# Optimization experiments

Hardware: AMD Instinct MI355X
Metric: run time of the kernel (lower is better)

## Reference

```python
import jax, jax.numpy as jnp
import numpy as np

N, E, D = 50000, 800000, 256

def setup_inputs() -> dict:
    key = jax.random.key(0)
    ks = jax.random.split(key, 12)
    s = 1.0 / np.sqrt(D)
    return {
        "x": jax.random.normal(ks[0], (N, D), dtype=jnp.float32),
        "src": jax.random.randint(ks[1], (E,), 0, N, dtype=jnp.int64),
        "dst": jax.random.randint(ks[2], (E,), 0, N, dtype=jnp.int64),
        "W_w": jax.random.normal(ks[3], (D, D), dtype=jnp.float32) * s,
        "W_b": jnp.zeros((D,), dtype=jnp.float32),
        "U_w": jax.random.normal(ks[4], (D, D), dtype=jnp.float32) * s,
        "U_b": jnp.zeros((D,), dtype=jnp.float32),
        "V_w": jax.random.normal(ks[5], (D, D), dtype=jnp.float32) * s,
        "V_b": jnp.zeros((D,), dtype=jnp.float32),
        "attn_l": jax.random.normal(ks[6], (D,), dtype=jnp.float32) * s,
        "attn_r": jax.random.normal(ks[7], (D,), dtype=jnp.float32) * s,
        "gamma": jnp.ones((D,), dtype=jnp.float32),
        "beta": jnp.zeros((D,), dtype=jnp.float32),
    }

def reference(x, src, dst, W_w, W_b, U_w, U_b, V_w, V_b, attn_l, attn_r, gamma, beta):
    # node transforms (dropout p=0 -> identity)
    Wh = x @ W_w + W_b            # [N, D]
    Uh = x @ U_w + U_b            # [N, D]
    Vh = x @ V_w + V_b            # [N, D]
    out_src = Wh * attn_l         # [N, D]
    out_dst = Wh * attn_r         # [N, D]
    # per-edge gate: sigma = sigmoid(out_src[u] + out_dst[v])  [E, D]
    sigma = jax.nn.sigmoid(out_src[src] + out_dst[dst])
    # aggregate to destination nodes
    sum_sigma_h = jax.ops.segment_sum(Vh[src] * sigma, dst, num_segments=N)
    sum_sigma = jax.ops.segment_sum(sigma, dst, num_segments=N)
    h = Uh + sum_sigma_h / (sum_sigma + 1e-6)
    # layer norm (eps=1e-6, affine)
    mu = jnp.mean(h, axis=-1, keepdims=True)
    var = jnp.mean((h - mu) ** 2, axis=-1, keepdims=True)
    h = (h - mu) / jnp.sqrt(var + 1e-6) * gamma + beta
    h = jax.nn.relu(h)
    return x + h  # residual
```

## Files before the change

### kernel.cpp

```cpp
#include <hip/hip_runtime.h>
#include <hip/hip_bf16.h>

#define NN 50000
#define NE 800000
#define NB 196

typedef __attribute__((ext_vector_type(8))) short short8;
typedef __attribute__((ext_vector_type(4))) float floatx4;
typedef unsigned short u16;
typedef unsigned int u32;

__device__ __forceinline__ u16 f2bf(float f) {
    u32 u = __float_as_uint(f);
    u += 0x7FFFu + ((u >> 16) & 1u);
    return (u16)(u >> 16);
}
__device__ __forceinline__ float bf_lo(u32 u) { return __uint_as_float(u << 16); }
__device__ __forceinline__ float bf_hi(u32 u) { return __uint_as_float(u & 0xFFFF0000u); }
__device__ __forceinline__ u32 pack_bf(float lo, float hi) {
    return (u32)f2bf(lo) | ((u32)f2bf(hi) << 16);
}
__device__ __forceinline__ void gl_lds16(const void* g, void* l) {
    __builtin_amdgcn_global_load_lds((const __attribute__((address_space(1))) void*)g,
                                     (__attribute__((address_space(3))) void*)l, 16, 0, 0);
}

__global__ __launch_bounds__(256) void tw_kernel(const float* __restrict__ W, const float* __restrict__ U,
                                                 const float* __restrict__ V, u16* __restrict__ wT) {
    __shared__ float s[32][33];
    int g = blockIdx.z;
    const float* M = (g == 0) ? W : ((g == 1) ? U : V);
    int r0 = blockIdx.x * 32, c0 = blockIdx.y * 32;
    int tx = threadIdx.x & 31, ty = threadIdx.x >> 5;
#pragma unroll
    for (int k = 0; k < 4; ++k)
        s[ty + k * 8][tx] = M[(size_t)(r0 + ty + k * 8) * 256 + c0 + tx];
    __syncthreads();
#pragma unroll
    for (int k = 0; k < 4; ++k)
        wT[(size_t)(g * 256 + c0 + ty + k * 8) * 256 + r0 + tx] = f2bf(s[tx][ty + k * 8]);
}

__global__ void hist_kernel(const int* __restrict__ dst, int* __restrict__ deg) {
    int e = blockIdx.x * 256 + threadIdx.x;
    if (e < NE) atomicAdd(&deg[dst[e]], 1);
}

__global__ __launch_bounds__(256) void scanA_kernel(const int* __restrict__ deg, int* __restrict__ bsum) {
    int t = threadIdx.x;
    int i = blockIdx.x * 256 + t;
    int v = (i < NN) ? deg[i] : 0;
#pragma unroll
    for (int m = 32; m; m >>= 1) v += __shfl_xor(v, m, 64);
    __shared__ int ws[4];
    if ((t & 63) == 0) ws[t >> 6] = v;
    __syncthreads();
    if (t == 0) bsum[blockIdx.x] = ws[0] + ws[1] + ws[2] + ws[3];
}

__global__ __launch_bounds__(256) void scanB_kernel(const int* __restrict__ bsum, int* __restrict__ bpre,
                                                    int* __restrict__ rows_end) {
    int t = threadIdx.x, lane = t & 63, wv = t >> 6;
    int v = (t < NB) ? bsum[t] : 0;
    int inc = v;
#pragma unroll
    for (int off = 1; off < 64; off <<= 1) {
        int u = __shfl_up(inc, off, 64);
        if (lane >= off) inc += u;
    }
    __shared__ int wsum[4];
    if (lane == 63) wsum[wv] = inc;
    __syncthreads();
    int woff = 0;
    for (int k = 0; k < wv; ++k) woff += wsum[k];
    if (t < NB) bpre[t] = woff + inc - v;
    if (t == 255) rows_end[0] = woff + inc;
}

__global__ __launch_bounds__(256) void scanC_kernel(const int* __restrict__ deg, const int* __restrict__ bpre,
                                                    int* __restrict__ rows, int* __restrict__ cursor) {
    int t = threadIdx.x, lane = t & 63, wv = t >> 6;
    int i = blockIdx.x * 256 + t;
    int v = (i < NN) ? deg[i] : 0;
    int inc = v;
#pragma unroll
    for (int off = 1; off < 64; off <<= 1) {
        int u = __shfl_up(inc, off, 64);
        if (lane >= off) inc += u;
    }
    __shared__ int wsum[4];
    if (lane == 63) wsum[wv] = inc;
    __syncthreads();
    int woff = bpre[blockIdx.x];
    for (int k = 0; k < wv; ++k) woff += wsum[k];
    int excl = woff + inc - v;
    if (i < NN) { rows[i] = excl; cursor[i] = excl; }
}

__global__ void scatter_kernel(const int* __restrict__ src, const int* __restrict__ dst,
                               int* __restrict__ cursor, int* __restrict__ esrc) {
    int e = blockIdx.x * 256 + threadIdx.x;
    if (e < NE) {
        int d = dst[e];
        int pos = atomicAdd(&cursor[d], 1);
        esrc[pos] = src[e];
    }
}

__global__ __launch_bounds__(256) void gemm_kernel(
    const float* __restrict__ x, const u16* __restrict__ wT,
    const float* __restrict__ Wb, const float* __restrict__ Ub, const float* __restrict__ Vb,
    u16* __restrict__ WVh, float* __restrict__ Uh) {
    __shared__ __align__(16) u16 As[128 * 64];
    __shared__ __align__(16) u16 Bs[128 * 64];

    int rb = blockIdx.x * 128;
    int cbg = blockIdx.y * 128;
    int t = threadIdx.x, lane = t & 63, w = t >> 6;
    int wm = w >> 1, wn = w & 1;

    floatx4 acc[4][4] = {};

    int b_subrow = lane >> 3;
    int b_q = lane & 7;
    int a_row = t >> 1;
    int a_half = t & 1;

    for (int kt = 0; kt < 4; ++kt) {
        int k0 = kt * 64;
#pragma unroll
        for (int ii = 0; ii < 4; ++ii) {
            int rowbase = (w * 4 + ii) * 8;
            int row = rowbase + b_subrow;
            int qa = b_q ^ (row & 7);
            gl_lds16(wT + (size_t)(cbg + row) * 256 + k0 + qa * 8, Bs + rowbase * 64);
        }
        int grow = rb + a_row;
        uint4 pk[4] = {};
        if (grow < NN) {
            const float* px = x + (size_t)grow * 256 + k0 + a_half * 32;
#pragma unroll
            for (int c = 0; c < 4; ++c) {
                floatx4 f0 = *(const floatx4*)(px + c * 8);
                floatx4 f1 = *(const floatx4*)(px + c * 8 + 4);
                pk[c].x = pack_bf(f0[0], f0[1]);
                pk[c].y = pack_bf(f0[2], f0[3]);
                pk[c].z = pack_bf(f1[0], f1[1]);
                pk[c].w = pack_bf(f1[2], f1[3]);
            }
        }
#pragma unroll
        for (int c = 0; c < 4; ++c) {
            int q = a_half * 4 + c;
            *(uint4*)(As + a_row * 64 + ((q ^ (a_row & 7)) * 8)) = pk[c];
        }
        __syncthreads();

#pragma unroll
        for (int s = 0; s < 2; ++s) {
            short8 a[4], b[4];
#pragma unroll
            for (int i = 0; i < 4; ++i) {
                int ar = wm * 64 + i * 16 + (lane & 15);
                int q = s * 4 + (lane >> 4);
                a[i] = *(const short8*)(As + ar * 64 + ((q ^ (ar & 7)) * 8));
                int br = wn * 64 + i * 16 + (lane & 15);
                b[i] = *(const short8*)(Bs + br * 64 + ((q ^ (br & 7)) * 8));
            }
#pragma unroll
            for (int i = 0; i < 4; ++i)
#pragma unroll
                for (int j = 0; j < 4; ++j)
                    acc[i][j] = __builtin_amdgcn_mfma_f32_16x16x32_bf16(a[i], b[j], acc[i][j], 0, 0, 0);
        }
        __syncthreads();
    }

    int g = cbg >> 8;
    int cloc = cbg & 255;
    const float* bias = (g == 0) ? Wb : ((g == 1) ? Ub : Vb);
#pragma unroll
    for (int i = 0; i < 4; ++i)
#pragma unroll
        for (int j = 0; j < 4; ++j) {
            int col = cloc + wn * 64 + j * 16 + (lane & 15);
            float bv = bias[col];
#pragma unroll
            for (int r = 0; r < 4; ++r) {
                int row = rb + wm * 64 + i * 16 + (lane >> 4) * 4 + r;
                if (row < NN) {
                    float val = acc[i][j][r] + bv;
                    if (g == 0)      WVh[(size_t)row * 512 + col] = f2bf(val);
                    else if (g == 1) Uh[(size_t)row * 256 + col] = val;
                    else             WVh[(size_t)row * 512 + 256 + col] = f2bf(val);
                }
            }
        }
}

__global__ __launch_bounds__(256) void node_kernel(
    const u16* __restrict__ WVh, const float* __restrict__ x,
    const int* __restrict__ rows, const int* __restrict__ esrc,
    const float* __restrict__ attn_l, const float* __restrict__ attn_r,
    const float* __restrict__ gamma, const float* __restrict__ beta,
    float* inout) {
    int wv = threadIdx.x >> 6, lane = threadIdx.x & 63;
    int v = blockIdx.x * 4 + wv;
    if (v >= NN) return;
    int c0 = lane * 4;

    floatx4 al = *(const floatx4*)(attn_l + c0);
    floatx4 ar = *(const floatx4*)(attn_r + c0);

    uint2 wvv = *(const uint2*)(WVh + (size_t)v * 512 + c0);
    float td[4] = { bf_lo(wvv.x) * ar[0], bf_hi(wvv.x) * ar[1],
                    bf_lo(wvv.y) * ar[2], bf_hi(wvv.y) * ar[3] };

    float acc_h[4] = {0.f, 0.f, 0.f, 0.f};
    float acc_s[4] = {0.f, 0.f, 0.f, 0.f};

    int e0 = rows[v], e1 = rows[v + 1];
    for (int e = e0; e < e1; ++e) {
        int u = esrc[e];
        const u16* base = WVh + (size_t)u * 512 + c0;
        uint2 wu = *(const uint2*)(base);
        uint2 vu = *(const uint2*)(base + 256);
        float wf[4] = { bf_lo(wu.x), bf_hi(wu.x), bf_lo(wu.y), bf_hi(wu.y) };
        float vf[4] = { bf_lo(vu.x), bf_hi(vu.x), bf_lo(vu.y), bf_hi(vu.y) };
#pragma unroll
        for (int j = 0; j < 4; ++j) {
            float tt = fmaf(wf[j], al[j], td[j]);
            float s = __builtin_amdgcn_rcpf(1.0f + __expf(-tt));
            acc_s[j] += s;
            acc_h[j] = fmaf(s, vf[j], acc_h[j]);
        }
    }

    floatx4 uh = *(const floatx4*)(inout + (size_t)v * 256 + c0);
    float h[4];
#pragma unroll
    for (int j = 0; j < 4; ++j)
        h[j] = uh[j] + acc_h[j] * __builtin_amdgcn_rcpf(acc_s[j] + 1e-6f);

    float s01 = h[0] + h[1] + h[2] + h[3];
#pragma unroll
    for (int m = 32; m; m >>= 1) s01 += __shfl_xor(s01, m, 64);
    float mu = s01 * (1.0f / 256.0f);
    float d[4] = { h[0] - mu, h[1] - mu, h[2] - mu, h[3] - mu };
    float sq = d[0] * d[0] + d[1] * d[1] + d[2] * d[2] + d[3] * d[3];
#pragma unroll
    for (int m = 32; m; m >>= 1) sq += __shfl_xor(sq, m, 64);
    float inv = rsqrtf(sq * (1.0f / 256.0f) + 1e-6f);

    floatx4 gm = *(const floatx4*)(gamma + c0);
    floatx4 bt = *(const floatx4*)(beta + c0);
    floatx4 xr = *(const floatx4*)(x + (size_t)v * 256 + c0);
    floatx4 res;
#pragma unroll
    for (int j = 0; j < 4; ++j) {
        float y = d[j] * inv * gm[j] + bt[j];
        y = fmaxf(y, 0.0f);
        res[j] = xr[j] + y;
    }
    *(floatx4*)(inout + (size_t)v * 256 + c0) = res;
}

extern "C" void kernel_launch(void* const* d_in, const int* in_sizes, int n_in,
                              void* d_out, int out_size, void* d_ws, size_t ws_size,
                              hipStream_t stream) {
    const float* x       = (const float*)d_in[0];
    const int*   src     = (const int*)d_in[1];
    const int*   dst     = (const int*)d_in[2];
    const float* W_w     = (const float*)d_in[3];
    const float* W_b     = (const float*)d_in[4];
    const float* U_w     = (const float*)d_in[5];
    const float* U_b     = (const float*)d_in[6];
    const float* V_w     = (const float*)d_in[7];
    const float* V_b     = (const float*)d_in[8];
    const float* attn_l  = (const float*)d_in[9];
    const float* attn_r  = (const float*)d_in[10];
    const float* gamma   = (const float*)d_in[11];
    const float* beta    = (const float*)d_in[12];

    char* ws = (char*)d_ws;
    size_t off = 0;
    auto alloc = [&](size_t bytes) -> char* {
        char* p = ws + off;
        off += (bytes + 255) & ~(size_t)255;
        return p;
    };
    u16* WVh     = (u16*)alloc((size_t)NN * 512 * 2);
    u16* wT      = (u16*)alloc((size_t)768 * 256 * 2);
    int* deg     = (int*)alloc((size_t)NN * 4);
    int* rows    = (int*)alloc((size_t)(NN + 1) * 4);
    int* cursor  = (int*)alloc((size_t)NN * 4);
    int* esrc    = (int*)alloc((size_t)NE * 4);
    int* bsum    = (int*)alloc((size_t)NB * 4);
    int* bpre    = (int*)alloc((size_t)NB * 4);

    float* Uh_f32 = (float*)d_out;

    hipMemsetAsync(deg, 0, (size_t)NN * 4, stream);

    tw_kernel<<<dim3(8, 8, 3), 256, 0, stream>>>(W_w, U_w, V_w, wT);
    hist_kernel<<<(NE + 255) / 256, 256, 0, stream>>>(dst, deg);
    scanA_kernel<<<NB, 256, 0, stream>>>(deg, bsum);
    scanB_kernel<<<1, 256, 0, stream>>>(bsum, bpre, rows + NN);
    scanC_kernel<<<NB, 256, 0, stream>>>(deg, bpre, rows, cursor);
    scatter_kernel<<<(NE + 255) / 256, 256, 0, stream>>>(src, dst, cursor, esrc);

    dim3 gg((NN + 127) / 128, 6);
    gemm_kernel<<<gg, 256, 0, stream>>>(x, wT, W_b, U_b, V_b, WVh, Uh_f32);

    node_kernel<<<(NN + 3) / 4, 256, 0, stream>>>(
        WVh, x, rows, esrc, attn_l, attn_r, gamma, beta, (float*)d_out);
}
```

Before: 339.3 us.

## Pre-convert x to bf16 for direct LDS loads and unroll edge gather

Adds a kernel that converts x to bf16 in a padded workspace buffer. The GEMM can then load A tiles straight into LDS with global_load_lds, the same way it loads the weights, instead of loading fp32 through registers and converting. It keeps the old fp32 GEMM as a fallback when the workspace is too small. Separately, the node kernel's edge loop is unrolled by four so several gathers are in flight at once, and the sigmoid argument is negated ahead of the loop. The cost is an extra pass over x plus a launch, and rows past NN in the padded buffer are read without being initialised.

```diff
diff --git a/kernel.cpp b/kernel.cpp
--- a/kernel.cpp
+++ b/kernel.cpp
@@ -4,6 +4,7 @@
 #define NN 50000
 #define NE 800000
 #define NB 196
+#define NROWPAD 50048
 
 typedef __attribute__((ext_vector_type(8))) short short8;
 typedef __attribute__((ext_vector_type(4))) float floatx4;
@@ -23,6 +24,18 @@
 __device__ __forceinline__ void gl_lds16(const void* g, void* l) {
     __builtin_amdgcn_global_load_lds((const __attribute__((address_space(1))) void*)g,
                                      (__attribute__((address_space(3))) void*)l, 16, 0, 0);
+}
+
+__global__ __launch_bounds__(256) void xcvt_kernel(const float* __restrict__ x, u16* __restrict__ xbf) {
+    size_t i = (size_t)(blockIdx.x * 256 + threadIdx.x) * 8;
+    floatx4 f0 = *(const floatx4*)(x + i);
+    floatx4 f1 = *(const floatx4*)(x + i + 4);
+    uint4 pk;
+    pk.x = pack_bf(f0[0], f0[1]);
+    pk.y = pack_bf(f0[2], f0[3]);
+    pk.z = pack_bf(f1[0], f1[1]);
+    pk.w = pack_bf(f1[2], f1[3]);
+    *(uint4*)(xbf + i) = pk;
 }
 
 __global__ __launch_bounds__(256) void tw_kernel(const float* __restrict__ W, const float* __restrict__ U,
@@ -107,7 +120,78 @@
     }
 }
 
-__global__ __launch_bounds__(256) void gemm_kernel(
+__global__ __launch_bounds__(256) void gemm_bf_kernel(
+    const u16* __restrict__ xbf, const u16* __restrict__ wT,
+    const float* __restrict__ Wb, const float* __restrict__ Ub, const float* __restrict__ Vb,
+    u16* __restrict__ WVh, float* __restrict__ Uh) {
+    __shared__ __align__(16) u16 As[128 * 64];
+    __shared__ __align__(16) u16 Bs[128 * 64];
+
+    int rb = blockIdx.x * 128;
+    int cbg = blockIdx.y * 128;
+    int t = threadIdx.x, lane = t & 63, w = t >> 6;
+    int wm = w >> 1, wn = w & 1;
+
+    floatx4 acc[4][4] = {};
+
+    int subrow = lane >> 3;
+    int qv = lane & 7;
+
+    for (int kt = 0; kt < 4; ++kt) {
+        int k0 = kt * 64;
+#pragma unroll
+        for (int ii = 0; ii < 4; ++ii) {
+            int rowbase = (w * 4 + ii) * 8;
+            int row = rowbase + subrow;
+            int qa = qv ^ (row & 7);
+            gl_lds16(wT + (size_t)(cbg + row) * 256 + k0 + qa * 8, Bs + rowbase * 64);
+            gl_lds16(xbf + (size_t)(rb + row) * 256 + k0 + qa * 8, As + rowbase * 64);
+        }
+        __syncthreads();
+
+#pragma unroll
+        for (int s = 0; s < 2; ++s) {
+            short8 a[4], b[4];
+#pragma unroll
+            for (int i = 0; i < 4; ++i) {
+                int ar = wm * 64 + i * 16 + (lane & 15);
+                int q = s * 4 + (lane >> 4);
+                a[i] = *(const short8*)(As + ar * 64 + ((q ^ (ar & 7)) * 8));
+                int br = wn * 64 + i * 16 + (lane & 15);
+                b[i] = *(const short8*)(Bs + br * 64 + ((q ^ (br & 7)) * 8));
+            }
+#pragma unroll
+            for (int i = 0; i < 4; ++i)
+#pragma unroll
+                for (int j = 0; j < 4; ++j)
+                    acc[i][j] = __builtin_amdgcn_mfma_f32_16x16x32_bf16(a[i], b[j], acc[i][j], 0, 0, 0);
+        }
+        __syncthreads();
+    }
+
+    int g = cbg >> 8;
+    int cloc = cbg & 255;
+    const float* bias = (g == 0) ? Wb : ((g == 1) ? Ub : Vb);
+#pragma unroll
+    for (int i = 0; i < 4; ++i)
+#pragma unroll
+        for (int j = 0; j < 4; ++j) {
+            int col = cloc + wn * 64 + j * 16 + (lane & 15);
+            float bv = bias[col];
+#pragma unroll
+            for (int r = 0; r < 4; ++r) {
+                int row = rb + wm * 64 + i * 16 + (lane >> 4) * 4 + r;
+                if (row < NN) {
+                    float val = acc[i][j][r] + bv;
+                    if (g == 0)      WVh[(size_t)row * 512 + col] = f2bf(val);
+                    else if (g == 1) Uh[(size_t)row * 256 + col] = val;
+                    else             WVh[(size_t)row * 512 + 256 + col] = f2bf(val);
+                }
+            }
+        }
+}
+
+__global__ __launch_bounds__(256) void gemm_f32_kernel(
     const float* __restrict__ x, const u16* __restrict__ wT,
     const float* __restrict__ Wb, const float* __restrict__ Ub, const float* __restrict__ Vb,
     u16* __restrict__ WVh, float* __restrict__ Uh) {
@@ -120,7 +204,6 @@
     int wm = w >> 1, wn = w & 1;
 
     floatx4 acc[4][4] = {};
-
     int b_subrow = lane >> 3;
     int b_q = lane & 7;
     int a_row = t >> 1;
@@ -209,31 +292,46 @@
     if (v >= NN) return;
     int c0 = lane * 4;
 
-    floatx4 al = *(const floatx4*)(attn_l + c0);
-    floatx4 ar = *(const floatx4*)(attn_r + c0);
-
+    floatx4 alv = *(const floatx4*)(attn_l + c0);
+    floatx4 arv = *(const floatx4*)(attn_r + c0);
     uint2 wvv = *(const uint2*)(WVh + (size_t)v * 512 + c0);
-    float td[4] = { bf_lo(wvv.x) * ar[0], bf_hi(wvv.x) * ar[1],
-                    bf_lo(wvv.y) * ar[2], bf_hi(wvv.y) * ar[3] };
+    float al2[4] = { -alv[0], -alv[1], -alv[2], -alv[3] };
+    float td2[4] = { -bf_lo(wvv.x) * arv[0], -bf_hi(wvv.x) * arv[1],
+                     -bf_lo(wvv.y) * arv[2], -bf_hi(wvv.y) * arv[3] };
 
     float acc_h[4] = {0.f, 0.f, 0.f, 0.f};
     float acc_s[4] = {0.f, 0.f, 0.f, 0.f};
 
-    int e0 = rows[v], e1 = rows[v + 1];
-    for (int e = e0; e < e1; ++e) {
-        int u = esrc[e];
-        const u16* base = WVh + (size_t)u * 512 + c0;
-        uint2 wu = *(const uint2*)(base);
-        uint2 vu = *(const uint2*)(base + 256);
+    auto edge = [&](uint2 wu, uint2 vu) {
         float wf[4] = { bf_lo(wu.x), bf_hi(wu.x), bf_lo(wu.y), bf_hi(wu.y) };
         float vf[4] = { bf_lo(vu.x), bf_hi(vu.x), bf_lo(vu.y), bf_hi(vu.y) };
 #pragma unroll
         for (int j = 0; j < 4; ++j) {
-            float tt = fmaf(wf[j], al[j], td[j]);
-            float s = __builtin_amdgcn_rcpf(1.0f + __expf(-tt));
+            float m = fmaf(wf[j], al2[j], td2[j]);
+            float s = __builtin_amdgcn_rcpf(1.0f + __expf(m));
             acc_s[j] += s;
             acc_h[j] = fmaf(s, vf[j], acc_h[j]);
         }
+    };
+
+    int e = rows[v], e1 = rows[v + 1];
+    for (; e + 4 <= e1; e += 4) {
+        int ua = esrc[e], ub = esrc[e + 1], uc = esrc[e + 2], ud = esrc[e + 3];
+        const u16* pa = WVh + (size_t)ua * 512 + c0;
+        const u16* pb = WVh + (size_t)ub * 512 + c0;
+        const u16* pc = WVh + (size_t)uc * 512 + c0;
+        const u16* pd = WVh + (size_t)ud * 512 + c0;
+        uint2 wa = *(const uint2*)pa, va = *(const uint2*)(pa + 256);
+        uint2 wb = *(const uint2*)pb, vb = *(const uint2*)(pb + 256);
+        uint2 wc = *(const uint2*)pc, vc = *(const uint2*)(pc + 256);
+        uint2 wd = *(const uint2*)pd, vd = *(const uint2*)(pd + 256);
+        edge(wa, va); edge(wb, vb); edge(wc, vc); edge(wd, vd);
+    }
+    for (; e < e1; ++e) {
+        int u = esrc[e];
+        const u16* p = WVh + (size_t)u * 512 + c0;
+        uint2 wu = *(const uint2*)p, vu = *(const uint2*)(p + 256);
+        edge(wu, vu);
     }
 
     floatx4 uh = *(const floatx4*)(inout + (size_t)v * 256 + c0);
@@ -297,6 +395,8 @@
     int* esrc    = (int*)alloc((size_t)NE * 4);
     int* bsum    = (int*)alloc((size_t)NB * 4);
     int* bpre    = (int*)alloc((size_t)NB * 4);
+    u16* xbf     = (u16*)alloc((size_t)NROWPAD * 256 * 2);
+    bool use_bf  = (ws_size >= off);
 
     float* Uh_f32 = (float*)d_out;
 
@@ -310,7 +410,12 @@
     scatter_kernel<<<(NE + 255) / 256, 256, 0, stream>>>(src, dst, cursor, esrc);
 
     dim3 gg((NN + 127) / 128, 6);
-    gemm_kernel<<<gg, 256, 0, stream>>>(x, wT, W_b, U_b, V_b, WVh, Uh_f32);
+    if (use_bf) {
+        xcvt_kernel<<<(NN * 256 / 8 + 255) / 256, 256, 0, stream>>>(x, xbf);
+        gemm_bf_kernel<<<gg, 256, 0, stream>>>(xbf, wT, W_b, U_b, V_b, WVh, Uh_f32);
+    } else {
+        gemm_f32_kernel<<<gg, 256, 0, stream>>>(x, wT, W_b, U_b, V_b, WVh, Uh_f32);
+    }
 
     node_kernel<<<(NN + 3) / 4, 256, 0, stream>>>(
         WVh, x, rows, esrc, attn_l, attn_r, gamma, beta, (float*)d_out);
```

After: 300.0 us. 11.6% less time.
